# Kernel optimization log

Measured on AMD Instinct MI355X. Metric: run time of the kernel, lower is better.

## Reference

```python
import jax, jax.numpy as jnp
import numpy as np

D = 64        # state dim (num_output)
H = 256       # MLP hidden width
B = 4096      # batch
NUM_STEPS = 16  # fixed-step Dormand-Prince steps over t in [0,1] per bijector


def _mlp(t, y, W1, b1, W2, b2, W3, b3):
    # time-conditioned MLP: concat scalar t to state, two tanh layers, linear out
    tcol = jnp.full((y.shape[0], 1), t, dtype=y.dtype)
    h = jnp.tanh(jnp.concatenate([y, tcol], axis=1) @ W1 + b1)
    h = jnp.tanh(h @ W2 + b2)
    return h @ W3 + b3


def _dopri5_fixed(f, y0):
    # classic Dormand-Prince (RK45) Butcher tableau, 5th-order solution,
    # fixed step h = 1/NUM_STEPS from t=0 to t=1
    h = jnp.asarray(1.0 / NUM_STEPS, dtype=y0.dtype)

    def step(y, i):
        t = i.astype(y0.dtype) * h
        k1 = f(t, y)
        k2 = f(t + h * (1/5),  y + h * ((1/5) * k1))
        k3 = f(t + h * (3/10), y + h * ((3/40) * k1 + (9/40) * k2))
        k4 = f(t + h * (4/5),  y + h * ((44/45) * k1 - (56/15) * k2 + (32/9) * k3))
        k5 = f(t + h * (8/9),  y + h * ((19372/6561) * k1 - (25360/2187) * k2
                                        + (64448/6561) * k3 - (212/729) * k4))
        k6 = f(t + h,          y + h * ((9017/3168) * k1 - (355/33) * k2
                                        + (46732/5247) * k3 + (49/176) * k4
                                        - (5103/18656) * k5))
        y_next = y + h * ((35/384) * k1 + (500/1113) * k3 + (125/192) * k4
                          - (2187/6784) * k5 + (11/84) * k6)
        return y_next, None

    y_final, _ = jax.lax.scan(step, y0, jnp.arange(NUM_STEPS))
    return y_final


def setup_inputs() -> dict:
    key = jax.random.key(0)
    ks = jax.random.split(key, 7)
    s_in = 1.0 / np.sqrt(D + 1)
    s_h = 1.0 / np.sqrt(H)
    inp = {"x": jax.random.normal(ks[0], (B, D), dtype=jnp.float32)}
    for i, base in enumerate([1, 4]):
        inp[f"p{i}_W1"] = jax.random.normal(ks[base], (D + 1, H), dtype=jnp.float32) * s_in
        inp[f"p{i}_b1"] = jnp.zeros((H,), dtype=jnp.float32)
        inp[f"p{i}_W2"] = jax.random.normal(ks[base + 1], (H, H), dtype=jnp.float32) * s_h
        inp[f"p{i}_b2"] = jnp.zeros((H,), dtype=jnp.float32)
        inp[f"p{i}_W3"] = jax.random.normal(ks[base + 2], (H, D), dtype=jnp.float32) * s_h
        inp[f"p{i}_b3"] = jnp.zeros((D,), dtype=jnp.float32)
    return inp


def reference(x, p0_W1, p0_b1, p0_W2, p0_b2, p0_W3, p0_b3,
              p1_W1, p1_b1, p1_W2, p1_b2, p1_W3, p1_b3):
    # Chain(list(reversed(bijectors))).forward applies bijector 0 first, then 1.
    # FFJORD bijector forward = integrate dz/dt = mlp(t, z) from t=0 to t=1.
    y = x
    params = [(p0_W1, p0_b1, p0_W2, p0_b2, p0_W3, p0_b3),
              (p1_W1, p1_b1, p1_W2, p1_b2, p1_W3, p1_b3)]
    for (W1, b1, W2, b2, W3, b3) in params:
        f = lambda t, z: _mlp(t, z, W1, b1, W2, b2, W3, b3)
        y = _dopri5_fixed(f, y)
    return y
```

## Files before the change

kernel.cpp:

```cpp
#include <hip/hip_runtime.h>

typedef __attribute__((ext_vector_type(8))) short short8;
typedef __attribute__((ext_vector_type(4))) float f32x4;

#define NSTEPS 16

__device__ __forceinline__ unsigned short bf16rne(float f) {
  unsigned int u = __float_as_uint(f);
  u += 0x7FFFu + ((u >> 16) & 1u);
  return (unsigned short)(u >> 16);
}

__device__ __forceinline__ unsigned int pk2(float a, float b) {
  unsigned int r;
  asm("v_cvt_pk_bf16_f32 %0, %1, %2" : "=v"(r) : "v"(a), "v"(b));
  return r;
}

__device__ __forceinline__ float tanh_fast(float x) {
  float e = __builtin_amdgcn_exp2f(x * 2.8853900817779268f);
  return __builtin_fmaf(-2.0f, __builtin_amdgcn_rcpf(e + 1.0f), 1.0f);
}

__global__ void ffjord_setup(const float* __restrict__ W1a, const float* __restrict__ W2a,
                             const float* __restrict__ W3a, const float* __restrict__ W1b,
                             const float* __restrict__ W2b, const float* __restrict__ W3b,
                             unsigned short* __restrict__ ws) {
  int gid = blockIdx.x * blockDim.x + threadIdx.x;
  int bij = gid / 12288;
  int r = gid - bij * 12288;
  const float* W1 = bij ? W1b : W1a;
  const float* W2 = bij ? W2b : W2a;
  const float* W3 = bij ? W3b : W3a;
  unsigned short* o = ws + bij * 98304;
  const float* src;
  int kstride;
  if (r < 2048) {
    int lane = r & 63, nt = (r >> 6) & 15, ks = r >> 10;
    int k0 = ks * 32 + (lane >> 4) * 8, n = nt * 16 + (lane & 15);
    src = W1 + k0 * 256 + n; kstride = 256; o += r * 8;
  } else if (r < 10240) {
    int rr = r - 2048;
    int lane = rr & 63, nt = (rr >> 6) & 15, ks = rr >> 10;
    int k0 = ks * 32 + (lane >> 4) * 8, n = nt * 16 + (lane & 15);
    src = W2 + k0 * 256 + n; kstride = 256; o += 16384 + rr * 8;
  } else {
    int rr = r - 10240;
    int lane = rr & 63, nt = (rr >> 6) & 3, ks = rr >> 8;
    int k0 = ks * 32 + (lane >> 4) * 8, n = nt * 16 + (lane & 15);
    src = W3 + k0 * 64 + n; kstride = 64; o += 81920 + rr * 8;
  }
  #pragma unroll
  for (int j = 0; j < 8; j++) o[j] = bf16rne(src[j * kstride]);
}

__global__ __launch_bounds__(1024, 4) void ffjord_main(
    const float* __restrict__ x, float* __restrict__ out,
    const unsigned short* __restrict__ ws,
    const float* __restrict__ W1a, const float* __restrict__ b1a,
    const float* __restrict__ b2a, const float* __restrict__ b3a,
    const float* __restrict__ W1b, const float* __restrict__ b1b,
    const float* __restrict__ b2b, const float* __restrict__ b3b) {
  __shared__ __align__(16) unsigned short zA[1088];
  __shared__ __align__(16) unsigned short h1A[4096];
  __shared__ __align__(16) unsigned short h2A[4096];
  __shared__ __align__(16) unsigned short w3s[2][16384];

  const int tid = threadIdx.x;
  const int wave = tid >> 6;
  const int lane = tid & 63;
  const int cl = lane & 15;
  const int qd = lane >> 4;
  const int row0 = blockIdx.x * 16;

  const int c0 = wave * 16 + qd * 4;
  const int hoff = (c0 >> 5) * 512 + ((c0 & 31) >> 3) * 128 + cl * 8 + (c0 & 7);
  const int zrb = qd * 136 + cl * 8;
  const int w3i = wave & 3;
  const int dl3 = w3i * 16 + qd * 4;
  const int zw = (2 * w3i + (qd >> 1)) * 136 + cl * 8 + 4 * (qd & 1);

  const float hstep = 1.0f / 16.0f;

  f32x4 yc;

  const float A2[5][5] = {
      {1.f / 5.f, 0.f, 0.f, 0.f, 0.f},
      {3.f / 40.f, 9.f / 40.f, 0.f, 0.f, 0.f},
      {44.f / 45.f, -56.f / 15.f, 32.f / 9.f, 0.f, 0.f},
      {19372.f / 6561.f, -25360.f / 2187.f, 64448.f / 6561.f, -212.f / 729.f, 0.f},
      {9017.f / 3168.f, -355.f / 33.f, 46732.f / 5247.f, 49.f / 176.f, -5103.f / 18656.f}};
  const float CT[6] = {0.0f, 0.2f, 0.3f, 0.8f, 8.0f / 9.0f, 1.0f};
  const float BW0 = 35.f / 384.f, BW2 = 500.f / 1113.f, BW3 = 125.f / 192.f,
              BW4 = -2187.f / 6784.f, BW5 = 11.f / 84.f;

  {
    const uint4* s0 = (const uint4*)(ws + 81920);
    const uint4* s1 = (const uint4*)(ws + 98304 + 81920);
    uint4* d0 = (uint4*)&w3s[0][0];
    uint4* d1 = (uint4*)&w3s[1][0];
    d0[tid] = s0[tid];
    d0[tid + 1024] = s0[tid + 1024];
    d1[tid] = s1[tid];
    d1[tid + 1024] = s1[tid + 1024];
  }

  for (int bij = 0; bij < 2; bij++) {
    const unsigned short* wsb = ws + bij * 98304;
    const float* W1 = bij ? W1b : W1a;
    const float* b1 = bij ? b1b : b1a;
    const float* b2 = bij ? b2b : b2a;
    const float* b3 = bij ? b3b : b3a;

    f32x4 b1c = *(const f32x4*)(b1 + c0);
    f32x4 w1t4 = *(const f32x4*)(W1 + 64 * 256 + c0);
    f32x4 b2c = *(const f32x4*)(b2 + c0);
    f32x4 b3c = *(const f32x4*)(b3 + dl3);

    const short8* w1p = (const short8*)wsb;
    const short8* w2p = (const short8*)(wsb + 16384);
    short8 w1f[2];
    #pragma unroll
    for (int ks = 0; ks < 2; ks++)
      w1f[ks] = w1p[(ks * 16 + wave) * 64 + lane];
    short8 w2f[8];
    #pragma unroll
    for (int ks = 0; ks < 8; ks++)
      w2f[ks] = w2p[(ks * 16 + wave) * 64 + lane];

    const short8* w3c = (const short8*)&w3s[bij][0];

    if (bij == 0 && wave < 4) {
      yc = *(const f32x4*)(x + (row0 + cl) * 64 + dl3);
      uint2 pv;
      pv.x = pk2(yc[0], yc[1]);
      pv.y = pk2(yc[2], yc[3]);
      *(uint2*)(zA + zw) = pv;
    }
    __syncthreads();

    for (int step = 0; step < NSTEPS; step++) {
      float stepf = (float)step;
      f32x4 kh[5];
      #pragma unroll
      for (int s = 0; s < 6; s++) {
        float ts = (stepf + CT[s]) * hstep;

        {
          short8 a0 = *(const short8*)(zA + zrb);
          short8 a1 = *(const short8*)(zA + zrb + 544);
          f32x4 acc;
          #pragma unroll
          for (int r = 0; r < 4; r++)
            acc[r] = __builtin_fmaf(ts, w1t4[r], b1c[r]);
          acc = __builtin_amdgcn_mfma_f32_16x16x32_bf16(w1f[0], a0, acc, 0, 0, 0);
          acc = __builtin_amdgcn_mfma_f32_16x16x32_bf16(w1f[1], a1, acc, 0, 0, 0);
          uint2 pv;
          pv.x = pk2(tanh_fast(acc[0]), tanh_fast(acc[1]));
          pv.y = pk2(tanh_fast(acc[2]), tanh_fast(acc[3]));
          *(uint2*)(h1A + hoff) = pv;
        }
        __syncthreads();

        {
          f32x4 accA = b2c;
          f32x4 accB; accB[0] = 0.f; accB[1] = 0.f; accB[2] = 0.f; accB[3] = 0.f;
          #pragma unroll
          for (int ks = 0; ks < 4; ks++) {
            short8 hb = ((const short8*)h1A)[ks * 64 + lane];
            accA = __builtin_amdgcn_mfma_f32_16x16x32_bf16(w2f[ks], hb, accA, 0, 0, 0);
          }
          #pragma unroll
          for (int ks = 4; ks < 8; ks++) {
            short8 hb = ((const short8*)h1A)[ks * 64 + lane];
            accB = __builtin_amdgcn_mfma_f32_16x16x32_bf16(w2f[ks], hb, accB, 0, 0, 0);
          }
          uint2 pv;
          pv.x = pk2(tanh_fast(accA[0] + accB[0]), tanh_fast(accA[1] + accB[1]));
          pv.y = pk2(tanh_fast(accA[2] + accB[2]), tanh_fast(accA[3] + accB[3]));
          *(uint2*)(h2A + hoff) = pv;
        }
        __syncthreads();

        if (wave < 4) {
          f32x4 accP = b3c;
          f32x4 accQ; accQ[0] = 0.f; accQ[1] = 0.f; accQ[2] = 0.f; accQ[3] = 0.f;
          #pragma unroll
          for (int ks = 0; ks < 8; ks += 2) {
            short8 hb0 = ((const short8*)h2A)[ks * 64 + lane];
            short8 wf0 = w3c[(ks * 4 + w3i) * 64 + lane];
            short8 hb1 = ((const short8*)h2A)[(ks + 1) * 64 + lane];
            short8 wf1 = w3c[((ks + 1) * 4 + w3i) * 64 + lane];
            accP = __builtin_amdgcn_mfma_f32_16x16x32_bf16(wf0, hb0, accP, 0, 0, 0);
            accQ = __builtin_amdgcn_mfma_f32_16x16x32_bf16(wf1, hb1, accQ, 0, 0, 0);
          }
          f32x4 kc;
          #pragma unroll
          for (int r = 0; r < 4; r++) kc[r] = accP[r] + accQ[r];

          f32x4 z;
          if (s < 5) {
            kh[s] = kc;
            #pragma unroll
            for (int r = 0; r < 4; r++)
              z[r] = __builtin_fmaf(hstep * A2[s][s], kc[r], yc[r]);
            #pragma unroll
            for (int j = 0; j < 4; j++)
              if (j < s) {
                float a = hstep * A2[s][j];
                #pragma unroll
                for (int r = 0; r < 4; r++) z[r] = __builtin_fmaf(a, kh[j][r], z[r]);
              }
          } else {
            #pragma unroll
            for (int r = 0; r < 4; r++) {
              float d = BW0 * kh[0][r] + BW2 * kh[2][r] + BW3 * kh[3][r] +
                        BW4 * kh[4][r] + BW5 * kc[r];
              yc[r] += hstep * d;
              z[r] = yc[r];
            }
          }
          uint2 pv;
          pv.x = pk2(z[0], z[1]);
          pv.y = pk2(z[2], z[3]);
          *(uint2*)(zA + zw) = pv;
        }
        __syncthreads();
      }
    }
  }

  if (wave < 4)
    *(f32x4*)(out + (row0 + cl) * 64 + dl3) = yc;
}

extern "C" void kernel_launch(void* const* d_in, const int* in_sizes, int n_in,
                              void* d_out, int out_size, void* d_ws, size_t ws_size,
                              hipStream_t stream) {
  (void)in_sizes; (void)n_in; (void)out_size; (void)ws_size;
  const float* x   = (const float*)d_in[0];
  const float* W1a = (const float*)d_in[1];
  const float* b1a = (const float*)d_in[2];
  const float* W2a = (const float*)d_in[3];
  const float* b2a = (const float*)d_in[4];
  const float* W3a = (const float*)d_in[5];
  const float* b3a = (const float*)d_in[6];
  const float* W1b = (const float*)d_in[7];
  const float* b1b = (const float*)d_in[8];
  const float* W2b = (const float*)d_in[9];
  const float* b2b = (const float*)d_in[10];
  const float* W3b = (const float*)d_in[11];
  const float* b3b = (const float*)d_in[12];
  unsigned short* ws = (unsigned short*)d_ws;
  float* out = (float*)d_out;

  hipLaunchKernelGGL(ffjord_setup, dim3(96), dim3(256), 0, stream,
                     W1a, W2a, W3a, W1b, W2b, W3b, ws);
  hipLaunchKernelGGL(ffjord_main, dim3(256), dim3(1024), 0, stream,
                     x, out, ws, W1a, b1a, b2a, b3a, W1b, b1b, b2b, b3b);
}
```

Measured before the change: 289.2 us.

## Halve block to 8 waves with two column tiles each, keep W3 in registers

The main kernel now launches 512 threads per block instead of 1024. Each wave computes two 16-column tiles of the hidden layers, so each wave holds twice as many W1/W2 fragments in registers. The W3 fragments move from LDS into registers for the first four waves, which drops the 64KB shared W3 copy and its per-block staging loads. Fewer waves per block means fewer waves arriving at each of the three barriers per stage, and the MFMA chains gain some independent work. The cost is higher register pressure per thread and less latency hiding from other waves.

```diff
diff --git a/kernel.cpp b/kernel.cpp
--- a/kernel.cpp
+++ b/kernel.cpp
@@ -54,7 +54,7 @@
   for (int j = 0; j < 8; j++) o[j] = bf16rne(src[j * kstride]);
 }
 
-__global__ __launch_bounds__(1024, 4) void ffjord_main(
+__global__ __launch_bounds__(512, 2) void ffjord_main(
     const float* __restrict__ x, float* __restrict__ out,
     const unsigned short* __restrict__ ws,
     const float* __restrict__ W1a, const float* __restrict__ b1a,
@@ -64,7 +64,6 @@
   __shared__ __align__(16) unsigned short zA[1088];
   __shared__ __align__(16) unsigned short h1A[4096];
   __shared__ __align__(16) unsigned short h2A[4096];
-  __shared__ __align__(16) unsigned short w3s[2][16384];
 
   const int tid = threadIdx.x;
   const int wave = tid >> 6;
@@ -73,8 +72,9 @@
   const int qd = lane >> 4;
   const int row0 = blockIdx.x * 16;
 
-  const int c0 = wave * 16 + qd * 4;
-  const int hoff = (c0 >> 5) * 512 + ((c0 & 31) >> 3) * 128 + cl * 8 + (c0 & 7);
+  const int tc0 = wave * 2, tc1 = tc0 + 1;
+  const int c0 = wave * 32 + qd * 4;
+  const int hoff = wave * 512 + (qd >> 1) * 128 + cl * 8 + 4 * (qd & 1);
   const int zrb = qd * 136 + cl * 8;
   const int w3i = wave & 3;
   const int dl3 = w3i * 16 + qd * 4;
@@ -94,17 +94,6 @@
   const float BW0 = 35.f / 384.f, BW2 = 500.f / 1113.f, BW3 = 125.f / 192.f,
               BW4 = -2187.f / 6784.f, BW5 = 11.f / 84.f;
 
-  {
-    const uint4* s0 = (const uint4*)(ws + 81920);
-    const uint4* s1 = (const uint4*)(ws + 98304 + 81920);
-    uint4* d0 = (uint4*)&w3s[0][0];
-    uint4* d1 = (uint4*)&w3s[1][0];
-    d0[tid] = s0[tid];
-    d0[tid + 1024] = s0[tid + 1024];
-    d1[tid] = s1[tid];
-    d1[tid + 1024] = s1[tid + 1024];
-  }
-
   for (int bij = 0; bij < 2; bij++) {
     const unsigned short* wsb = ws + bij * 98304;
     const float* W1 = bij ? W1b : W1a;
@@ -112,23 +101,35 @@
     const float* b2 = bij ? b2b : b2a;
     const float* b3 = bij ? b3b : b3a;
 
-    f32x4 b1c = *(const f32x4*)(b1 + c0);
-    f32x4 w1t4 = *(const f32x4*)(W1 + 64 * 256 + c0);
-    f32x4 b2c = *(const f32x4*)(b2 + c0);
+    f32x4 b1c0 = *(const f32x4*)(b1 + c0);
+    f32x4 b1c1 = *(const f32x4*)(b1 + c0 + 16);
+    f32x4 w1t0 = *(const f32x4*)(W1 + 64 * 256 + c0);
+    f32x4 w1t1 = *(const f32x4*)(W1 + 64 * 256 + c0 + 16);
+    f32x4 b2c0 = *(const f32x4*)(b2 + c0);
+    f32x4 b2c1 = *(const f32x4*)(b2 + c0 + 16);
     f32x4 b3c = *(const f32x4*)(b3 + dl3);
 
     const short8* w1p = (const short8*)wsb;
     const short8* w2p = (const short8*)(wsb + 16384);
-    short8 w1f[2];
+    const short8* w3p = (const short8*)(wsb + 81920);
+    short8 w1f0[2], w1f1[2];
     #pragma unroll
-    for (int ks = 0; ks < 2; ks++)
-      w1f[ks] = w1p[(ks * 16 + wave) * 64 + lane];
-    short8 w2f[8];
+    for (int ks = 0; ks < 2; ks++) {
+      w1f0[ks] = w1p[(ks * 16 + tc0) * 64 + lane];
+      w1f1[ks] = w1p[(ks * 16 + tc1) * 64 + lane];
+    }
+    short8 w2f0[8], w2f1[8];
     #pragma unroll
-    for (int ks = 0; ks < 8; ks++)
-      w2f[ks] = w2p[(ks * 16 + wave) * 64 + lane];
-
-    const short8* w3c = (const short8*)&w3s[bij][0];
+    for (int ks = 0; ks < 8; ks++) {
+      w2f0[ks] = w2p[(ks * 16 + tc0) * 64 + lane];
+      w2f1[ks] = w2p[(ks * 16 + tc1) * 64 + lane];
+    }
+    short8 w3f[8];
+    if (wave < 4) {
+      #pragma unroll
+      for (int ks = 0; ks < 8; ks++)
+        w3f[ks] = w3p[(ks * 4 + w3i) * 64 + lane];
+    }
 
     if (bij == 0 && wave < 4) {
       yc = *(const f32x4*)(x + (row0 + cl) * 64 + dl3);
@@ -149,36 +150,49 @@
         {
           short8 a0 = *(const short8*)(zA + zrb);
           short8 a1 = *(const short8*)(zA + zrb + 544);
-          f32x4 acc;
-          #pragma unroll
-          for (int r = 0; r < 4; r++)
-            acc[r] = __builtin_fmaf(ts, w1t4[r], b1c[r]);
-          acc = __builtin_amdgcn_mfma_f32_16x16x32_bf16(w1f[0], a0, acc, 0, 0, 0);
-          acc = __builtin_amdgcn_mfma_f32_16x16x32_bf16(w1f[1], a1, acc, 0, 0, 0);
-          uint2 pv;
-          pv.x = pk2(tanh_fast(acc[0]), tanh_fast(acc[1]));
-          pv.y = pk2(tanh_fast(acc[2]), tanh_fast(acc[3]));
-          *(uint2*)(h1A + hoff) = pv;
+          f32x4 acc0, acc1;
+          #pragma unroll
+          for (int r = 0; r < 4; r++) {
+            acc0[r] = __builtin_fmaf(ts, w1t0[r], b1c0[r]);
+            acc1[r] = __builtin_fmaf(ts, w1t1[r], b1c1[r]);
+          }
+          acc0 = __builtin_amdgcn_mfma_f32_16x16x32_bf16(w1f0[0], a0, acc0, 0, 0, 0);
+          acc1 = __builtin_amdgcn_mfma_f32_16x16x32_bf16(w1f1[0], a0, acc1, 0, 0, 0);
+          acc0 = __builtin_amdgcn_mfma_f32_16x16x32_bf16(w1f0[1], a1, acc0, 0, 0, 0);
+          acc1 = __builtin_amdgcn_mfma_f32_16x16x32_bf16(w1f1[1], a1, acc1, 0, 0, 0);
+          uint2 pv0, pv1;
+          pv0.x = pk2(tanh_fast(acc0[0]), tanh_fast(acc0[1]));
+          pv0.y = pk2(tanh_fast(acc0[2]), tanh_fast(acc0[3]));
+          pv1.x = pk2(tanh_fast(acc1[0]), tanh_fast(acc1[1]));
+          pv1.y = pk2(tanh_fast(acc1[2]), tanh_fast(acc1[3]));
+          *(uint2*)(h1A + hoff) = pv0;
+          *(uint2*)(h1A + hoff + 256) = pv1;
         }
         __syncthreads();
 
         {
-          f32x4 accA = b2c;
-          f32x4 accB; accB[0] = 0.f; accB[1] = 0.f; accB[2] = 0.f; accB[3] = 0.f;
+          f32x4 aA0 = b2c0, aA1 = b2c1;
+          f32x4 aB0; aB0[0] = 0.f; aB0[1] = 0.f; aB0[2] = 0.f; aB0[3] = 0.f;
+          f32x4 aB1 = aB0;
           #pragma unroll
           for (int ks = 0; ks < 4; ks++) {
             short8 hb = ((const short8*)h1A)[ks * 64 + lane];
-            accA = __builtin_amdgcn_mfma_f32_16x16x32_bf16(w2f[ks], hb, accA, 0, 0, 0);
+            aA0 = __builtin_amdgcn_mfma_f32_16x16x32_bf16(w2f0[ks], hb, aA0, 0, 0, 0);
+            aA1 = __builtin_amdgcn_mfma_f32_16x16x32_bf16(w2f1[ks], hb, aA1, 0, 0, 0);
           }
           #pragma unroll
           for (int ks = 4; ks < 8; ks++) {
             short8 hb = ((const short8*)h1A)[ks * 64 + lane];
-            accB = __builtin_amdgcn_mfma_f32_16x16x32_bf16(w2f[ks], hb, accB, 0, 0, 0);
-          }
-          uint2 pv;
-          pv.x = pk2(tanh_fast(accA[0] + accB[0]), tanh_fast(accA[1] + accB[1]));
-          pv.y = pk2(tanh_fast(accA[2] + accB[2]), tanh_fast(accA[3] + accB[3]));
-          *(uint2*)(h2A + hoff) = pv;
+            aB0 = __builtin_amdgcn_mfma_f32_16x16x32_bf16(w2f0[ks], hb, aB0, 0, 0, 0);
+            aB1 = __builtin_amdgcn_mfma_f32_16x16x32_bf16(w2f1[ks], hb, aB1, 0, 0, 0);
+          }
+          uint2 pv0, pv1;
+          pv0.x = pk2(tanh_fast(aA0[0] + aB0[0]), tanh_fast(aA0[1] + aB0[1]));
+          pv0.y = pk2(tanh_fast(aA0[2] + aB0[2]), tanh_fast(aA0[3] + aB0[3]));
+          pv1.x = pk2(tanh_fast(aA1[0] + aB1[0]), tanh_fast(aA1[1] + aB1[1]));
+          pv1.y = pk2(tanh_fast(aA1[2] + aB1[2]), tanh_fast(aA1[3] + aB1[3]));
+          *(uint2*)(h2A + hoff) = pv0;
+          *(uint2*)(h2A + hoff + 256) = pv1;
         }
         __syncthreads();
 
@@ -188,11 +202,9 @@
           #pragma unroll
           for (int ks = 0; ks < 8; ks += 2) {
             short8 hb0 = ((const short8*)h2A)[ks * 64 + lane];
-            short8 wf0 = w3c[(ks * 4 + w3i) * 64 + lane];
             short8 hb1 = ((const short8*)h2A)[(ks + 1) * 64 + lane];
-            short8 wf1 = w3c[((ks + 1) * 4 + w3i) * 64 + lane];
-            accP = __builtin_amdgcn_mfma_f32_16x16x32_bf16(wf0, hb0, accP, 0, 0, 0);
-            accQ = __builtin_amdgcn_mfma_f32_16x16x32_bf16(wf1, hb1, accQ, 0, 0, 0);
+            accP = __builtin_amdgcn_mfma_f32_16x16x32_bf16(w3f[ks], hb0, accP, 0, 0, 0);
+            accQ = __builtin_amdgcn_mfma_f32_16x16x32_bf16(w3f[ks + 1], hb1, accQ, 0, 0, 0);
           }
           f32x4 kc;
           #pragma unroll
@@ -256,6 +268,6 @@
 
   hipLaunchKernelGGL(ffjord_setup, dim3(96), dim3(256), 0, stream,
                      W1a, W2a, W3a, W1b, W2b, W3b, ws);
-  hipLaunchKernelGGL(ffjord_main, dim3(256), dim3(1024), 0, stream,
+  hipLaunchKernelGGL(ffjord_main, dim3(256), dim3(512), 0, stream,
                      x, out, ws, W1a, b1a, b2a, b3a, W1b, b1b, b2b, b3b);
 }
```

Result: slower. 298.9 us (+3.4%).
